# Kernel tuning notes

Measured on AMD Instinct MI355X. Metric: run time of the kernel, lower is better.

Reference implementation:

```python
import jax, jax.numpy as jnp
import numpy as np


def setup_inputs() -> dict:
    key = jax.random.key(0)
    k1, k2, k3 = jax.random.split(key, 3)
    B, S, D, L = 8, 512, 512, 32
    head = jax.random.normal(k1, (B, S, D), dtype=jnp.float32)
    dep = jax.random.normal(k2, (B, S, D), dtype=jnp.float32)
    label_U_diag = jax.random.normal(k3, (L, D), dtype=jnp.float32)
    return {"head": head, "dep": dep, "label_U_diag": label_U_diag}


def reference(head, dep, label_U_diag):
    # head: [b, i, j], label_U_diag: [l, j], dep: [b, o, j] -> [b, l, i, o]
    return jnp.einsum('bij,lj,boj->blio', head, label_U_diag, dep)
```

## Files before the change

kernel.cpp:

```cpp
#include <hip/hip_runtime.h>
#include <hip/hip_bf16.h>

typedef float f32x4  __attribute__((ext_vector_type(4)));
typedef short bf16x8 __attribute__((ext_vector_type(8)));

__device__ __forceinline__ short bf16r(float x) {
    unsigned u = __builtin_bit_cast(unsigned, x);
    u += 0x7fffu + ((u >> 16) & 1u);
    return (short)(u >> 16);
}

__global__ void cvt_kernel(const float* __restrict__ head, const float* __restrict__ dep,
                           short* __restrict__ hb, short* __restrict__ db) {
    const int n8 = 8 * 512 * 512 / 8;
    int i = blockIdx.x * blockDim.x + threadIdx.x;
    const float* src = (i < n8) ? head : dep;
    short* dst = (i < n8) ? hb : db;
    int j = (i < n8) ? i : i - n8;
    f32x4 a = *(const f32x4*)(src + (size_t)j * 8);
    f32x4 c = *(const f32x4*)(src + (size_t)j * 8 + 4);
    bf16x8 v;
#pragma unroll
    for (int e = 0; e < 4; ++e) { v[e] = bf16r(a[e]); v[4 + e] = bf16r(c[e]); }
    *(bf16x8*)(dst + (size_t)j * 8) = v;
}

__global__ __launch_bounds__(256, 2)
void bla_gemm9(const short* __restrict__ headb,
               const short* __restrict__ depb,
               const float* __restrict__ U,
               float* __restrict__ out)
{
    constexpr int S = 512, D = 512, L = 32, BM = 128, BN = 128, BK = 64, NT = 8;

    __shared__ __align__(16) short Al[2][BM * BK];
    __shared__ __align__(16) short Bl[2][BN * BK];
    __shared__ __align__(16) float Ul[2][512];

    const int tid = threadIdx.x, lane = tid & 63, wid = tid >> 6;
    const int wm = wid >> 1, wn = wid & 1;

    const int swz = (blockIdx.x & 7) * ((int)gridDim.x >> 3) + (blockIdx.x >> 3);
    const int b = swz >> 8, rem = swz & 255;
    const int it = rem >> 6, ot = (rem >> 4) & 3, lp = rem & 15;
    const int i0 = it * BM, o0 = ot * BN, l0 = lp * 2;

    const int bso = ((lane & 7) * 16) ^ ((lane >> 3) << 4);
    const char* asrc = (const char*)(headb + (size_t)(b * S + i0) * D) + bso;
    const char* bsrc = (const char*)(depb + (size_t)(b * S + o0) * D) + bso;

#define SB()  __builtin_amdgcn_sched_barrier(0)
#define BAR() __builtin_amdgcn_s_barrier()

#define A_GLOAD(tt) do {                                                        \
        _Pragma("unroll")                                                       \
        for (int q = 0; q < 4; ++q) {                                           \
            const int rg = wid * 32 + q * 8 + (lane >> 3);                      \
            __builtin_amdgcn_global_load_lds(                                   \
                (const __attribute__((address_space(1))) void*)(asrc +          \
                    ((size_t)rg * D + (size_t)(tt) * BK) * 2),                  \
                (__attribute__((address_space(3))) void*)                       \
                    (&Al[(tt) & 1][(wid * 32 + q * 8) * BK] + lane * 8),        \
                16, 0, 0);                                                      \
        }                                                                       \
    } while (0)

#define B_GLOAD(tt) do {                                                        \
        _Pragma("unroll")                                                       \
        for (int q = 0; q < 4; ++q) {                                           \
            const int rg = wid * 32 + q * 8 + (lane >> 3);                      \
            __builtin_amdgcn_global_load_lds(                                   \
                (const __attribute__((address_space(1))) void*)(bsrc +          \
                    ((size_t)rg * D + (size_t)(tt) * BK) * 2),                  \
                (__attribute__((address_space(3))) void*)                       \
                    (&Bl[(tt) & 1][(wid * 32 + q * 8) * BK] + lane * 8),        \
                16, 0, 0);                                                      \
        }                                                                       \
    } while (0)

    f32x4 acc0[4][4] = {}, acc1[4][4] = {};
    bf16x8 af[4], bfr[4], av[4];
    f32x4 uf[2][2][2];

#define DSREAD_A(buf_, ks_) do {                                                \
        const int cb = (ks_) * 64 + ((lane >> 4) << 4);                         \
        _Pragma("unroll")                                                       \
        for (int f = 0; f < 4; ++f) {                                           \
            const int row = wm * 64 + f * 16 + (lane & 15);                     \
            af[f] = *(const bf16x8*)&Al[buf_][row * BK + ((cb ^ ((row & 7) << 4)) >> 1)]; \
        }                                                                       \
    } while (0)

#define DSREAD_B(buf_, ks_) do {                                                \
        const int cb = (ks_) * 64 + ((lane >> 4) << 4);                         \
        _Pragma("unroll")                                                       \
        for (int f = 0; f < 4; ++f) {                                           \
            const int row = wn * 64 + f * 16 + (lane & 15);                     \
            bfr[f] = *(const bf16x8*)&Bl[buf_][row * BK + ((cb ^ ((row & 7) << 4)) >> 1)]; \
        }                                                                       \
    } while (0)

#define UF_READ(tt) do {                                                        \
        _Pragma("unroll")                                                       \
        for (int li = 0; li < 2; ++li)                                          \
            _Pragma("unroll")                                                   \
            for (int ks = 0; ks < 2; ++ks)                                      \
                _Pragma("unroll")                                               \
                for (int h = 0; h < 2; ++h)                                     \
                    uf[li][ks][h] = *(const f32x4*)&Ul[li][(tt) * 64 + ks * 32  \
                        + ((lane >> 4) << 3) + h * 4];                          \
    } while (0)

#define SCALE(li_, ks_) do {                                                    \
        _Pragma("unroll")                                                       \
        for (int mf = 0; mf < 4; ++mf) {                                        \
            bf16x8 t_;                                                          \
            _Pragma("unroll")                                                   \
            for (int e = 0; e < 8; ++e) {                                       \
                float f = __builtin_bit_cast(float,                             \
                    (unsigned)((unsigned short)af[mf][e]) << 16)                \
                    * uf[li_][ks_][e >> 2][e & 3];                              \
                t_[e] = __builtin_bit_cast(short, __float2bfloat16(f));         \
            }                                                                   \
            av[mf] = t_;                                                        \
        }                                                                       \
    } while (0)

#define MFMA16(accX) do {                                                       \
        _Pragma("unroll")                                                       \
        for (int m = 0; m < 4; ++m)                                             \
            _Pragma("unroll")                                                   \
            for (int n = 0; n < 4; ++n)                                         \
                accX[m][n] = __builtin_amdgcn_mfma_f32_16x16x32_bf16(           \
                    av[m], bfr[n], accX[m][n], 0, 0, 0);                        \
    } while (0)

    {
        const int li = tid >> 7, idx = (tid & 127) * 4;
        *(f32x4*)&Ul[li][idx] = *(const f32x4*)&U[(size_t)(l0 + li) * D + idx];
    }
    A_GLOAD(0);
    B_GLOAD(0);
    asm volatile("s_waitcnt vmcnt(0) lgkmcnt(0)" ::: "memory");
    SB();
    BAR();

#pragma unroll
    for (int t = 0; t < NT; ++t) {
        const int c = t & 1;

        UF_READ(t);
        if (t + 1 < NT) { A_GLOAD(t + 1); B_GLOAD(t + 1); }
        DSREAD_A(c, 0); DSREAD_B(c, 0);
        SCALE(0, 0); MFMA16(acc0);
        SCALE(1, 0); MFMA16(acc1);
        DSREAD_A(c, 1); DSREAD_B(c, 1);
        SCALE(0, 1); MFMA16(acc0);
        SCALE(1, 1); MFMA16(acc1);
        if (t + 1 < NT) {
            asm volatile("s_waitcnt vmcnt(0)" ::: "memory");
            SB();
            BAR();
        }
    }

#pragma unroll
    for (int li = 0; li < 2; ++li) {
        float* op = out + (size_t)(b * L + l0 + li) * S * S;
#pragma unroll
        for (int m = 0; m < 4; ++m) {
            const int row0 = i0 + wm * 64 + m * 16 + ((lane >> 4) << 2);
#pragma unroll
            for (int n = 0; n < 4; ++n) {
                const int col = o0 + wn * 64 + n * 16 + (lane & 15);
#pragma unroll
                for (int r = 0; r < 4; ++r)
                    op[(size_t)(row0 + r) * S + col] =
                        li ? acc1[m][n][r] : acc0[m][n][r];
            }
        }
    }

#undef SB
#undef BAR
#undef A_GLOAD
#undef B_GLOAD
#undef DSREAD_A
#undef DSREAD_B
#undef UF_READ
#undef SCALE
#undef MFMA16
}

__global__ __launch_bounds__(256, 2)
void bla_fb(const float* __restrict__ head, const float* __restrict__ dep,
            const float* __restrict__ U, float* __restrict__ out)
{
    constexpr int S = 512, D = 512, L = 32, BM = 128, BN = 128, BK = 64, NT = 8;
    __shared__ short Al[2][BM * BK];
    __shared__ short Bl[2][BN * BK];
    const int tid = threadIdx.x, lane = tid & 63, wid = tid >> 6;
    const int wm = wid >> 1, wn = wid & 1;
    const int swz = (blockIdx.x & 7) * ((int)gridDim.x >> 3) + (blockIdx.x >> 3);
    const int b = swz >> 9, rem = swz & 511;
    const int l = rem >> 4, it = (rem >> 2) & 3, ot = rem & 3;
    const int i0 = it * BM, o0 = ot * BN;
    const int srow = tid >> 3, scol = (tid & 7) * 8, swb = scol * 2;
    const float* hb = head + (size_t)(b * S + i0 + srow) * D + scol;
    const float* db = dep + (size_t)(b * S + o0 + srow) * D + scol;
    const float* ub = U + l * D + scol;
    f32x4 ra[4][2], rb[4][2], ru[2];
#define FSTAGE_LOAD(t) do { const int k0_ = (t) * BK;                              \
        ru[0] = *(const f32x4*)(ub + k0_); ru[1] = *(const f32x4*)(ub + k0_ + 4);  \
        _Pragma("unroll") for (int p_ = 0; p_ < 4; ++p_) {                         \
            ra[p_][0] = *(const f32x4*)(hb + k0_ + p_ * 32 * D);                   \
            ra[p_][1] = *(const f32x4*)(hb + k0_ + p_ * 32 * D + 4);               \
            rb[p_][0] = *(const f32x4*)(db + k0_ + p_ * 32 * D);                   \
            rb[p_][1] = *(const f32x4*)(db + k0_ + p_ * 32 * D + 4); } } while (0)
#define FSTAGE_WRITE(buf) do { _Pragma("unroll") for (int p_ = 0; p_ < 4; ++p_) {  \
            const int row_ = srow + p_ * 32; const int sb_ = swb ^ ((row_ & 7) << 4); \
            bf16x8 av_, bv_;                                                       \
            _Pragma("unroll") for (int q_ = 0; q_ < 2; ++q_)                       \
                _Pragma("unroll") for (int j_ = 0; j_ < 4; ++j_) {                 \
                    av_[q_ * 4 + j_] = bf16r(ra[p_][q_][j_] * ru[q_][j_]);         \
                    bv_[q_ * 4 + j_] = bf16r(rb[p_][q_][j_]); }                    \
            *(bf16x8*)&Al[buf][row_ * BK + (sb_ >> 1)] = av_;                      \
            *(bf16x8*)&Bl[buf][row_ * BK + (sb_ >> 1)] = bv_; } } while (0)
    f32x4 acc[4][4] = {};
    const int cbase = (lane >> 4) << 4, rsw = (lane & 7) << 4;
#define FCOMPUTE(buf) do { _Pragma("unroll") for (int ks_ = 0; ks_ < 2; ++ks_) {   \
            const int sb2_ = (ks_ * 64 + cbase) ^ rsw; bf16x8 af_[4], bfr_[4];     \
            _Pragma("unroll") for (int f_ = 0; f_ < 4; ++f_) {                     \
                af_[f_] = *(const bf16x8*)&Al[buf][(wm * 64 + f_ * 16 + (lane & 15)) * BK + (sb2_ >> 1)]; \
                bfr_[f_] = *(const bf16x8*)&Bl[buf][(wn * 64 + f_ * 16 + (lane & 15)) * BK + (sb2_ >> 1)]; } \
            _Pragma("unroll") for (int fm_ = 0; fm_ < 4; ++fm_)                    \
                _Pragma("unroll") for (int fn_ = 0; fn_ < 4; ++fn_)                \
                    acc[fm_][fn_] = __builtin_amdgcn_mfma_f32_16x16x32_bf16(       \
                        af_[fm_], bfr_[fn_], acc[fm_][fn_], 0, 0, 0); } } while (0)
    FSTAGE_LOAD(0); FSTAGE_WRITE(0); __syncthreads();
    int cur = 0;
#pragma unroll
    for (int t = 0; t < NT; ++t) {
        if (t + 1 < NT) FSTAGE_LOAD(t + 1);
        FCOMPUTE(cur);
        if (t + 1 < NT) FSTAGE_WRITE(cur ^ 1);
        __syncthreads();
        cur ^= 1;
    }
    float* op = out + (size_t)(b * L + l) * S * S;
#pragma unroll
    for (int fm = 0; fm < 4; ++fm) {
        const int row0 = i0 + wm * 64 + fm * 16 + ((lane >> 4) << 2);
#pragma unroll
        for (int fn = 0; fn < 4; ++fn) {
            const int col = o0 + wn * 64 + fn * 16 + (lane & 15);
#pragma unroll
            for (int r = 0; r < 4; ++r)
                op[(size_t)(row0 + r) * S + col] = acc[fm][fn][r];
        }
    }
#undef FSTAGE_LOAD
#undef FSTAGE_WRITE
#undef FCOMPUTE
}

extern "C" void kernel_launch(void* const* d_in, const int* in_sizes, int n_in,
                              void* d_out, int out_size, void* d_ws, size_t ws_size,
                              hipStream_t stream)
{
    const float* head = (const float*)d_in[0];
    const float* dep  = (const float*)d_in[1];
    const float* U    = (const float*)d_in[2];
    float* out        = (float*)d_out;

    const size_t nelem = (size_t)8 * 512 * 512;
    const size_t need  = nelem * 2 * 2;
    if (ws_size >= need) {
        short* headb = (short*)d_ws;
        short* depb  = headb + nelem;
        cvt_kernel<<<dim3(2048), dim3(256), 0, stream>>>(head, dep, headb, depb);
        bla_gemm9<<<dim3(2048), dim3(256), 0, stream>>>(headb, depb, U, out);
    } else {
        bla_fb<<<dim3(4096), dim3(256), 0, stream>>>(head, dep, U, out);
    }
}
```

Measured before the change: 127.6 us.

## Pre-pack operands into MFMA fragment layout and load directly to registers

The conversion kernel now writes bf16 head/dep in a fragment-major packed layout (16-row blocks by 8-element k-chunks) so each lane's MFMA operand is one contiguous 16-byte global load. The GEMM drops LDS staging, barriers and swizzled ds_reads, and instead double-buffers operand and U-scale registers straight from global memory, issuing loads two k-steps ahead. This removes LDS traffic and block-level synchronisation. In exchange, operand reuse across waves now depends on L1/L2 rather than shared memory, and register pressure rises.

```diff
diff --git a/kernel.cpp b/kernel.cpp
--- a/kernel.cpp
+++ b/kernel.cpp
@@ -10,32 +10,33 @@
     return (short)(u >> 16);
 }
 
-__global__ void cvt_kernel(const float* __restrict__ head, const float* __restrict__ dep,
-                           short* __restrict__ hb, short* __restrict__ db) {
-    const int n8 = 8 * 512 * 512 / 8;
-    int i = blockIdx.x * blockDim.x + threadIdx.x;
-    const float* src = (i < n8) ? head : dep;
-    short* dst = (i < n8) ? hb : db;
-    int j = (i < n8) ? i : i - n8;
-    f32x4 a = *(const f32x4*)(src + (size_t)j * 8);
-    f32x4 c = *(const f32x4*)(src + (size_t)j * 8 + 4);
+__global__ void pack_kernel(const float* __restrict__ head, const float* __restrict__ dep,
+                            short* __restrict__ hp, short* __restrict__ dp) {
+    const int per = 8 * 512 * 64;
+    int gid = blockIdx.x * blockDim.x + threadIdx.x;
+    const float* src = (gid < per) ? head : dep;
+    short* dst = (gid < per) ? hp : dp;
+    int g = (gid < per) ? gid : gid - per;
+    const int r  = g & 15;
+    const int j8 = (g >> 4) & 63;
+    const int ib = (g >> 10) & 31;
+    const int b  = g >> 15;
+    const float* s = src + ((size_t)(b * 512 + ib * 16 + r)) * 512 + j8 * 8;
+    f32x4 a = *(const f32x4*)s;
+    f32x4 c = *(const f32x4*)(s + 4);
     bf16x8 v;
 #pragma unroll
     for (int e = 0; e < 4; ++e) { v[e] = bf16r(a[e]); v[4 + e] = bf16r(c[e]); }
-    *(bf16x8*)(dst + (size_t)j * 8) = v;
+    *(bf16x8*)(dst + ((((size_t)(b * 32 + ib)) * 64 + j8) * 16 + r) * 8) = v;
 }
 
 __global__ __launch_bounds__(256, 2)
-void bla_gemm9(const short* __restrict__ headb,
-               const short* __restrict__ depb,
-               const float* __restrict__ U,
-               float* __restrict__ out)
+void bla_gemm11(const short* __restrict__ hp,
+                const short* __restrict__ dp,
+                const float* __restrict__ U,
+                float* __restrict__ out)
 {
-    constexpr int S = 512, D = 512, L = 32, BM = 128, BN = 128, BK = 64, NT = 8;
-
-    __shared__ __align__(16) short Al[2][BM * BK];
-    __shared__ __align__(16) short Bl[2][BN * BK];
-    __shared__ __align__(16) float Ul[2][512];
+    constexpr int S = 512, L = 32, NT = 16;
 
     const int tid = threadIdx.x, lane = tid & 63, wid = tid >> 6;
     const int wm = wid >> 1, wn = wid & 1;
@@ -43,126 +44,73 @@
     const int swz = (blockIdx.x & 7) * ((int)gridDim.x >> 3) + (blockIdx.x >> 3);
     const int b = swz >> 8, rem = swz & 255;
     const int it = rem >> 6, ot = (rem >> 4) & 3, lp = rem & 15;
-    const int i0 = it * BM, o0 = ot * BN, l0 = lp * 2;
-
-    const int bso = ((lane & 7) * 16) ^ ((lane >> 3) << 4);
-    const char* asrc = (const char*)(headb + (size_t)(b * S + i0) * D) + bso;
-    const char* bsrc = (const char*)(depb + (size_t)(b * S + o0) * D) + bso;
-
-#define SB()  __builtin_amdgcn_sched_barrier(0)
-#define BAR() __builtin_amdgcn_s_barrier()
-
-#define A_GLOAD(tt) do {                                                        \
-        _Pragma("unroll")                                                       \
-        for (int q = 0; q < 4; ++q) {                                           \
-            const int rg = wid * 32 + q * 8 + (lane >> 3);                      \
-            __builtin_amdgcn_global_load_lds(                                   \
-                (const __attribute__((address_space(1))) void*)(asrc +          \
-                    ((size_t)rg * D + (size_t)(tt) * BK) * 2),                  \
-                (__attribute__((address_space(3))) void*)                       \
-                    (&Al[(tt) & 1][(wid * 32 + q * 8) * BK] + lane * 8),        \
-                16, 0, 0);                                                      \
-        }                                                                       \
+    const int i0 = it * 128, o0 = ot * 128, l0 = lp * 2;
+
+    const short* abase = hp + (((size_t)(b * 32 + (i0 >> 4) + wm * 4)) * 64
+                               + (lane >> 4)) * 128 + (lane & 15) * 8;
+    const short* bbase = dp + (((size_t)(b * 32 + (o0 >> 4) + wn * 4)) * 64
+                               + (lane >> 4)) * 128 + (lane & 15) * 8;
+    const float* u0 = U + (size_t)l0 * 512 + ((lane >> 4) << 3);
+    const float* u1 = u0 + 512;
+
+    bf16x8 ra[2][4], rb[2][4];
+    f32x4  ru[2][2][2];
+    f32x4  acc0[4][4] = {}, acc1[4][4] = {};
+
+#define ISSUE(t_) do {                                                          \
+        const int p_ = (t_) & 1;                                                \
+        _Pragma("unroll")                                                       \
+        for (int m = 0; m < 4; ++m)                                             \
+            ra[p_][m] = *(const bf16x8*)(abase + m * 8192 + (t_) * 512);        \
+        _Pragma("unroll")                                                       \
+        for (int n = 0; n < 4; ++n)                                             \
+            rb[p_][n] = *(const bf16x8*)(bbase + n * 8192 + (t_) * 512);        \
+        ru[p_][0][0] = *(const f32x4*)(u0 + (t_) * 32);                         \
+        ru[p_][0][1] = *(const f32x4*)(u0 + (t_) * 32 + 4);                     \
+        ru[p_][1][0] = *(const f32x4*)(u1 + (t_) * 32);                         \
+        ru[p_][1][1] = *(const f32x4*)(u1 + (t_) * 32 + 4);                     \
     } while (0)
 
-#define B_GLOAD(tt) do {                                                        \
-        _Pragma("unroll")                                                       \
-        for (int q = 0; q < 4; ++q) {                                           \
-            const int rg = wid * 32 + q * 8 + (lane >> 3);                      \
-            __builtin_amdgcn_global_load_lds(                                   \
-                (const __attribute__((address_space(1))) void*)(bsrc +          \
-                    ((size_t)rg * D + (size_t)(tt) * BK) * 2),                  \
-                (__attribute__((address_space(3))) void*)                       \
-                    (&Bl[(tt) & 1][(wid * 32 + q * 8) * BK] + lane * 8),        \
-                16, 0, 0);                                                      \
-        }                                                                       \
-    } while (0)
-
-    f32x4 acc0[4][4] = {}, acc1[4][4] = {};
-    bf16x8 af[4], bfr[4], av[4];
-    f32x4 uf[2][2][2];
-
-#define DSREAD_A(buf_, ks_) do {                                                \
-        const int cb = (ks_) * 64 + ((lane >> 4) << 4);                         \
-        _Pragma("unroll")                                                       \
-        for (int f = 0; f < 4; ++f) {                                           \
-            const int row = wm * 64 + f * 16 + (lane & 15);                     \
-            af[f] = *(const bf16x8*)&Al[buf_][row * BK + ((cb ^ ((row & 7) << 4)) >> 1)]; \
-        }                                                                       \
-    } while (0)
-
-#define DSREAD_B(buf_, ks_) do {                                                \
-        const int cb = (ks_) * 64 + ((lane >> 4) << 4);                         \
-        _Pragma("unroll")                                                       \
-        for (int f = 0; f < 4; ++f) {                                           \
-            const int row = wn * 64 + f * 16 + (lane & 15);                     \
-            bfr[f] = *(const bf16x8*)&Bl[buf_][row * BK + ((cb ^ ((row & 7) << 4)) >> 1)]; \
-        }                                                                       \
-    } while (0)
-
-#define UF_READ(tt) do {                                                        \
-        _Pragma("unroll")                                                       \
-        for (int li = 0; li < 2; ++li)                                          \
-            _Pragma("unroll")                                                   \
-            for (int ks = 0; ks < 2; ++ks)                                      \
-                _Pragma("unroll")                                               \
-                for (int h = 0; h < 2; ++h)                                     \
-                    uf[li][ks][h] = *(const f32x4*)&Ul[li][(tt) * 64 + ks * 32  \
-                        + ((lane >> 4) << 3) + h * 4];                          \
-    } while (0)
-
-#define SCALE(li_, ks_) do {                                                    \
-        _Pragma("unroll")                                                       \
-        for (int mf = 0; mf < 4; ++mf) {                                        \
-            bf16x8 t_;                                                          \
+#define STEP(t_) do {                                                           \
+        const int p_ = (t_) & 1;                                                \
+        _Pragma("unroll")                                                       \
+        for (int m = 0; m < 4; ++m) {                                           \
+            bf16x8 av;                                                          \
             _Pragma("unroll")                                                   \
             for (int e = 0; e < 8; ++e) {                                       \
                 float f = __builtin_bit_cast(float,                             \
-                    (unsigned)((unsigned short)af[mf][e]) << 16)                \
-                    * uf[li_][ks_][e >> 2][e & 3];                              \
-                t_[e] = __builtin_bit_cast(short, __float2bfloat16(f));         \
+                    (unsigned)((unsigned short)ra[p_][m][e]) << 16)             \
+                    * ru[p_][0][e >> 2][e & 3];                                 \
+                av[e] = __builtin_bit_cast(short, __float2bfloat16(f));         \
             }                                                                   \
-            av[mf] = t_;                                                        \
+            _Pragma("unroll")                                                   \
+            for (int n = 0; n < 4; ++n)                                         \
+                acc0[m][n] = __builtin_amdgcn_mfma_f32_16x16x32_bf16(           \
+                    av, rb[p_][n], acc0[m][n], 0, 0, 0);                        \
         }                                                                       \
+        _Pragma("unroll")                                                       \
+        for (int m = 0; m < 4; ++m) {                                           \
+            bf16x8 av;                                                          \
+            _Pragma("unroll")                                                   \
+            for (int e = 0; e < 8; ++e) {                                       \
+                float f = __builtin_bit_cast(float,                             \
+                    (unsigned)((unsigned short)ra[p_][m][e]) << 16)             \
+                    * ru[p_][1][e >> 2][e & 3];                                 \
+                av[e] = __builtin_bit_cast(short, __float2bfloat16(f));         \
+            }                                                                   \
+            _Pragma("unroll")                                                   \
+            for (int n = 0; n < 4; ++n)                                         \
+                acc1[m][n] = __builtin_amdgcn_mfma_f32_16x16x32_bf16(           \
+                    av, rb[p_][n], acc1[m][n], 0, 0, 0);                        \
+        }                                                                       \
+        if ((t_) + 2 < NT) ISSUE((t_) + 2);                                     \
     } while (0)
 
-#define MFMA16(accX) do {                                                       \
-        _Pragma("unroll")                                                       \
-        for (int m = 0; m < 4; ++m)                                             \
-            _Pragma("unroll")                                                   \
-            for (int n = 0; n < 4; ++n)                                         \
-                accX[m][n] = __builtin_amdgcn_mfma_f32_16x16x32_bf16(           \
-                    av[m], bfr[n], accX[m][n], 0, 0, 0);                        \
-    } while (0)
-
-    {
-        const int li = tid >> 7, idx = (tid & 127) * 4;
-        *(f32x4*)&Ul[li][idx] = *(const f32x4*)&U[(size_t)(l0 + li) * D + idx];
-    }
-    A_GLOAD(0);
-    B_GLOAD(0);
-    asm volatile("s_waitcnt vmcnt(0) lgkmcnt(0)" ::: "memory");
-    SB();
-    BAR();
-
-#pragma unroll
-    for (int t = 0; t < NT; ++t) {
-        const int c = t & 1;
-
-        UF_READ(t);
-        if (t + 1 < NT) { A_GLOAD(t + 1); B_GLOAD(t + 1); }
-        DSREAD_A(c, 0); DSREAD_B(c, 0);
-        SCALE(0, 0); MFMA16(acc0);
-        SCALE(1, 0); MFMA16(acc1);
-        DSREAD_A(c, 1); DSREAD_B(c, 1);
-        SCALE(0, 1); MFMA16(acc0);
-        SCALE(1, 1); MFMA16(acc1);
-        if (t + 1 < NT) {
-            asm volatile("s_waitcnt vmcnt(0)" ::: "memory");
-            SB();
-            BAR();
-        }
-    }
+    ISSUE(0);
+    ISSUE(1);
+#pragma unroll
+    for (int t = 0; t < NT; ++t)
+        STEP(t);
 
 #pragma unroll
     for (int li = 0; li < 2; ++li) {
@@ -181,15 +129,8 @@
         }
     }
 
-#undef SB
-#undef BAR
-#undef A_GLOAD
-#undef B_GLOAD
-#undef DSREAD_A
-#undef DSREAD_B
-#undef UF_READ
-#undef SCALE
-#undef MFMA16
+#undef ISSUE
+#undef STEP
 }
 
 __global__ __launch_bounds__(256, 2)
@@ -276,10 +217,10 @@
     const size_t nelem = (size_t)8 * 512 * 512;
     const size_t need  = nelem * 2 * 2;
     if (ws_size >= need) {
-        short* headb = (short*)d_ws;
-        short* depb  = headb + nelem;
-        cvt_kernel<<<dim3(2048), dim3(256), 0, stream>>>(head, dep, headb, depb);
-        bla_gemm9<<<dim3(2048), dim3(256), 0, stream>>>(headb, depb, U, out);
+        short* hp = (short*)d_ws;
+        short* dp = hp + nelem;
+        pack_kernel<<<dim3(2048), dim3(256), 0, stream>>>(head, dep, hp, dp);
+        bla_gemm11<<<dim3(2048), dim3(256), 0, stream>>>(hp, dp, U, out);
     } else {
         bla_fb<<<dim3(4096), dim3(256), 0, stream>>>(head, dep, U, out);
     }
```

Measured after the change: 147.0 us. 15.2% more time.
